# Optimization experiments

Hardware: AMD Instinct MI355X
Metric: run time of the kernel (lower is better)

The kernel has to match this reference:

```python
import math
import jax, jax.numpy as jnp
import numpy as np

DIM = 1280
NUM_HEADS = 16
HEAD_DIM = DIM // NUM_HEADS  # 80
N_SEG = 8
SEG_LEN = 1024
TOTAL = N_SEG * SEG_LEN  # 8192


def setup_inputs() -> dict:
    key = jax.random.key(0)
    ks = jax.random.split(key, 6)
    hidden_states = jax.random.normal(ks[0], (TOTAL, DIM), dtype=jnp.float32)
    # equal-length packed segments (8 images x 1024 patches)
    cu_seqlens = jnp.arange(N_SEG + 1, dtype=jnp.int32) * SEG_LEN
    rotary_pos_emb = jax.random.uniform(ks[1], (TOTAL, HEAD_DIM // 2), dtype=jnp.float32) * (2.0 * math.pi)
    s = 0.02
    qkv_w = jax.random.normal(ks[2], (DIM, 3 * DIM), dtype=jnp.float32) * s
    qkv_b = jnp.zeros((3 * DIM,), dtype=jnp.float32)
    proj_w = jax.random.normal(ks[3], (DIM, DIM), dtype=jnp.float32) * s
    proj_b = jnp.zeros((DIM,), dtype=jnp.float32)
    return {
        "hidden_states": hidden_states,
        "rotary_pos_emb": rotary_pos_emb,
        "qkv_w": qkv_w,
        "qkv_b": qkv_b,
        "proj_w": proj_w,
        "proj_b": proj_b,
        "cu_seqlens": cu_seqlens,
    }


def _rotate_half(x):
    d = x.shape[-1] // 2
    return jnp.concatenate([-x[..., d:], x[..., :d]], axis=-1)


def _apply_rope(t, freqs):
    # t: [S, H, D] ; freqs: [S, D/2]
    orig = t.dtype
    tf = t.astype(jnp.float32)
    cos = jnp.tile(jnp.cos(freqs), (1, 2))[:, None, :].astype(jnp.float32)  # [S,1,D]
    sin = jnp.tile(jnp.sin(freqs), (1, 2))[:, None, :].astype(jnp.float32)
    return (tf * cos + _rotate_half(tf) * sin).astype(orig)


def reference(hidden_states, rotary_pos_emb, qkv_w, qkv_b, proj_w, proj_b, cu_seqlens):
    S, dim = hidden_states.shape
    H, D = NUM_HEADS, HEAD_DIM
    n_seg = cu_seqlens.shape[0] - 1  # static
    L = S // n_seg  # equal-length segments

    qkv = hidden_states @ qkv_w + qkv_b            # [S, 3*dim]
    qkv = qkv.reshape(S, 3, H, D)
    q, k, v = qkv[:, 0], qkv[:, 1], qkv[:, 2]      # [S, H, D]

    q = _apply_rope(q, rotary_pos_emb)
    k = _apply_rope(k, rotary_pos_emb)

    # block-diagonal (per-segment) attention, vectorized over segments
    qs = q.reshape(n_seg, L, H, D).transpose(0, 2, 1, 3)  # [G,H,L,D]
    ks = k.reshape(n_seg, L, H, D).transpose(0, 2, 1, 3)
    vs = v.reshape(n_seg, L, H, D).transpose(0, 2, 1, 3)

    scale = 1.0 / math.sqrt(D)
    scores = jnp.einsum("ghld,ghmd->ghlm", qs, ks) * scale       # [G,H,L,L]
    probs = jax.nn.softmax(scores.astype(jnp.float32), axis=-1).astype(qs.dtype)
    out = jnp.einsum("ghlm,ghmd->ghld", probs, vs)               # [G,H,L,D]
    out = out.transpose(0, 2, 1, 3).reshape(S, H * D)            # [S, dim]
    return out @ proj_w + proj_b
```

## Files before the change

kernel.cpp:

```cpp
#include <hip/hip_runtime.h>
#include <hip/hip_bf16.h>
#include <math.h>

#define DIM 1280
#define NHEADS 16
#define HD 80
#define HDP 96
#define NSEG 8
#define SEGLEN 1024
#define TOTAL (NSEG*SEGLEN)

typedef unsigned short u16;
typedef __attribute__((ext_vector_type(8))) short bf16x8;
typedef __attribute__((ext_vector_type(4))) float f32x4;

__device__ __forceinline__ u16 f2b(float f) {
    union { float f; unsigned int i; } v; v.f = f;
    unsigned int x = v.i;
    unsigned int r = x + 0x7FFFu + ((x >> 16) & 1u);
    return (u16)(r >> 16);
}
__device__ __forceinline__ float b2f(u16 u) {
    union { unsigned int i; float f; } v; v.i = ((unsigned int)u) << 16;
    return v.f;
}
__device__ __forceinline__ void gload16(const u16* g, u16* l) {
    __builtin_amdgcn_global_load_lds(
        (const __attribute__((address_space(1))) unsigned int*)g,
        (__attribute__((address_space(3))) unsigned int*)l, 16, 0, 0);
}

__global__ __launch_bounds__(256) void cvt_f32_bf16(const float* __restrict__ in,
                                                    u16* __restrict__ out, int n4) {
    int i = blockIdx.x * 256 + threadIdx.x;
    if (i >= n4) return;
    float4 a = ((const float4*)in)[i];
    u16 o[4] = { f2b(a.x), f2b(a.y), f2b(a.z), f2b(a.w) };
    *(ulong1*)&out[i*4] = *(ulong1*)o;
}

__global__ __launch_bounds__(256) void cvtT_w(const float* __restrict__ in,
                                              u16* __restrict__ out, int K, int N) {
    __shared__ float t[32][33];
    const int kb = blockIdx.x * 32, nb = blockIdx.y * 32;
    const int tx = threadIdx.x & 31, ty = threadIdx.x >> 5;
    #pragma unroll
    for (int i = 0; i < 4; ++i) {
        int r = i*8 + ty;
        t[r][tx] = in[(size_t)(kb + r)*N + nb + tx];
    }
    __syncthreads();
    #pragma unroll
    for (int i = 0; i < 4; ++i) {
        int n = i*8 + ty;
        out[(size_t)(nb + n)*K + kb + tx] = f2b(t[tx][n]);
    }
}

__global__ __launch_bounds__(256) void ctab_build(const float* __restrict__ rp,
                                                  float2* __restrict__ cs) {
    int i = blockIdx.x * 256 + threadIdx.x;
    if (i >= TOTAL*40) return;
    float s, c;
    sincosf(rp[i], &s, &c);
    cs[i] = make_float2(c, s);
}

template<int MODE>
__global__ __launch_bounds__(512, 2) void gemm8p(
    const u16* __restrict__ A, const u16* __restrict__ BT,
    const float* __restrict__ bias,
    float* __restrict__ Cf, u16* __restrict__ qo, u16* __restrict__ ko,
    u16* __restrict__ vo, int M, int N, int K, int nbx)
{
    __shared__ u16 sA[2][256*64];
    __shared__ u16 sB[2][256*64];

    const int tid = threadIdx.x;
    const int w = tid >> 6, l = tid & 63;
    const int lq = l & 15, lg = l >> 4;
    const int wm = w >> 2, wn = w & 3;

    const int nwg = gridDim.x;
    const int q8 = nwg >> 3;
    const int id = blockIdx.x;
    const int id2 = (id & 7) * q8 + (id >> 3);
    const int bx = id2 % nbx, by = id2 / nbx;
    const int brow = by * 256, bcol = bx * 256;

    const int rlo  = w*8 + (l >> 3);
    const int srcc = (l & 7) ^ ((l >> 3) & 7);
    const size_t aBase = (size_t)(brow + rlo)*K + srcc*8;
    const size_t bBase = (size_t)(bcol + rlo)*K + srcc*8;

    const int cx0 = (0 + lg) ^ (lq & 7);
    const int cx1 = (4 + lg) ^ (lq & 7);

    f32x4 acc[8][4] = {};
    const int NT = K >> 6;

    u16* cA = &sA[0][0]; u16* cB = &sB[0][0];
    u16* nA = &sA[1][0]; u16* nB = &sB[1][0];

    #pragma unroll
    for (int ci = 0; ci < 4; ++ci) {
        gload16(A  + aBase + (size_t)(ci*64)*K, &cA[(ci*512 + w*64)*8]);
        gload16(BT + bBase + (size_t)(ci*64)*K, &cB[(ci*512 + w*64)*8]);
    }
    asm volatile("s_waitcnt vmcnt(0)" ::: "memory");
    __builtin_amdgcn_s_barrier();

    for (int t = 0; t < NT; ++t) {
        const bool pf = (t + 1 < NT);
        const int kb = (t + 1) << 6;
        bf16x8 af[4], bf[4];

        if (pf) {
            gload16(A  + aBase + (size_t)(0*64)*K + kb, &nA[(0*512 + w*64)*8]);
            gload16(A  + aBase + (size_t)(2*64)*K + kb, &nA[(2*512 + w*64)*8]);
            gload16(BT + bBase + (size_t)(0*64)*K + kb, &nB[(0*512 + w*64)*8]);
        }
        #pragma unroll
        for (int n = 0; n < 4; ++n)
            bf[n] = *(const bf16x8*)&cB[(wn*64 + n*16 + lq)*64 + cx0*8];
        #pragma unroll
        for (int mi = 0; mi < 4; ++mi)
            af[mi] = *(const bf16x8*)&cA[(wm*128 + mi*16 + lq)*64 + cx0*8];
        __builtin_amdgcn_s_barrier();
        __builtin_amdgcn_s_setprio(1);
        #pragma unroll
        for (int mi = 0; mi < 4; ++mi)
            #pragma unroll
            for (int n = 0; n < 4; ++n)
                acc[mi][n] = __builtin_amdgcn_mfma_f32_16x16x32_bf16(af[mi], bf[n], acc[mi][n], 0, 0, 0);
        __builtin_amdgcn_s_setprio(0);
        __builtin_amdgcn_s_barrier();

        if (pf) {
            gload16(A  + aBase + (size_t)(1*64)*K + kb, &nA[(1*512 + w*64)*8]);
            gload16(A  + aBase + (size_t)(3*64)*K + kb, &nA[(3*512 + w*64)*8]);
            gload16(BT + bBase + (size_t)(1*64)*K + kb, &nB[(1*512 + w*64)*8]);
        }
        #pragma unroll
        for (int mi = 0; mi < 4; ++mi)
            af[mi] = *(const bf16x8*)&cA[(wm*128 + 64 + mi*16 + lq)*64 + cx0*8];
        __builtin_amdgcn_s_barrier();
        __builtin_amdgcn_s_setprio(1);
        #pragma unroll
        for (int mi = 0; mi < 4; ++mi)
            #pragma unroll
            for (int n = 0; n < 4; ++n)
                acc[4+mi][n] = __builtin_amdgcn_mfma_f32_16x16x32_bf16(af[mi], bf[n], acc[4+mi][n], 0, 0, 0);
        __builtin_amdgcn_s_setprio(0);
        __builtin_amdgcn_s_barrier();

        if (pf) {
            gload16(BT + bBase + (size_t)(2*64)*K + kb, &nB[(2*512 + w*64)*8]);
            gload16(BT + bBase + (size_t)(3*64)*K + kb, &nB[(3*512 + w*64)*8]);
        }
        #pragma unroll
        for (int n = 0; n < 4; ++n)
            bf[n] = *(const bf16x8*)&cB[(wn*64 + n*16 + lq)*64 + cx1*8];
        #pragma unroll
        for (int mi = 0; mi < 4; ++mi)
            af[mi] = *(const bf16x8*)&cA[(wm*128 + mi*16 + lq)*64 + cx1*8];
        __builtin_amdgcn_s_barrier();
        __builtin_amdgcn_s_setprio(1);
        #pragma unroll
        for (int mi = 0; mi < 4; ++mi)
            #pragma unroll
            for (int n = 0; n < 4; ++n)
                acc[mi][n] = __builtin_amdgcn_mfma_f32_16x16x32_bf16(af[mi], bf[n], acc[mi][n], 0, 0, 0);
        __builtin_amdgcn_s_setprio(0);
        __builtin_amdgcn_s_barrier();

        #pragma unroll
        for (int mi = 0; mi < 4; ++mi)
            af[mi] = *(const bf16x8*)&cA[(wm*128 + 64 + mi*16 + lq)*64 + cx1*8];
        __builtin_amdgcn_s_barrier();
        __builtin_amdgcn_s_setprio(1);
        #pragma unroll
        for (int mi = 0; mi < 4; ++mi)
            #pragma unroll
            for (int n = 0; n < 4; ++n)
                acc[4+mi][n] = __builtin_amdgcn_mfma_f32_16x16x32_bf16(af[mi], bf[n], acc[4+mi][n], 0, 0, 0);
        __builtin_amdgcn_s_setprio(0);
        if (pf) asm volatile("s_waitcnt vmcnt(0)" ::: "memory");
        __builtin_amdgcn_s_barrier();

        u16* tA = cA; cA = nA; nA = tA;
        u16* tB = cB; cB = nB; nB = tB;
    }

    #pragma unroll
    for (int mf = 0; mf < 8; ++mf) {
        #pragma unroll
        for (int n = 0; n < 4; ++n) {
            const int col = bcol + wn*64 + n*16 + lq;
            const float bv = bias[col];
            #pragma unroll
            for (int r = 0; r < 4; ++r) {
                const int row = brow + wm*128 + mf*16 + lg*4 + r;
                float val = acc[mf][n][r] + bv;
                if (MODE == 0) {
                    Cf[(size_t)row*N + col] = val;
                } else {
                    int part = col / DIM, rem = col - part*DIM;
                    int hh = rem / HD, dd = rem - hh*HD;
                    int g = row >> 10, ll = row & 1023;
                    size_t tok = (size_t)((g*NHEADS + hh)*SEGLEN + ll);
                    if      (part == 0) qo[tok*HDP + dd] = f2b(val);
                    else if (part == 1) ko[tok*HDP + dd] = f2b(val);
                    else                vo[tok*HD  + dd] = f2b(val);
                }
            }
        }
    }
}

__global__ __launch_bounds__(256) void rope_pad2(u16* __restrict__ qb, u16* __restrict__ kb,
                                                 const float2* __restrict__ cs)
{
    int idx = blockIdx.x * 256 + threadIdx.x;
    int l = idx & 1023, h = (idx >> 10) & 15, g = idx >> 14;
    size_t base = ((size_t)((g*NHEADS + h)*SEGLEN + l)) * HDP;
    const float2* c0 = cs + (size_t)(g*SEGLEN + l) * 40;
    #pragma unroll
    for (int p = 0; p < 5; ++p) {
        float cv[8], sv[8];
        #pragma unroll
        for (int j2 = 0; j2 < 4; ++j2) {
            float4 f = ((const float4*)(c0 + p*8))[j2];
            cv[j2*2] = f.x; sv[j2*2] = f.y; cv[j2*2+1] = f.z; sv[j2*2+1] = f.w;
        }
        bf16x8 qlo = *(const bf16x8*)&qb[base + p*8];
        bf16x8 qhi = *(const bf16x8*)&qb[base + 40 + p*8];
        bf16x8 klo = *(const bf16x8*)&kb[base + p*8];
        bf16x8 khi = *(const bf16x8*)&kb[base + 40 + p*8];
        bf16x8 qlo2, qhi2, klo2, khi2;
        #pragma unroll
        for (int j = 0; j < 8; ++j) {
            float a  = b2f((u16)qlo[j]), b  = b2f((u16)qhi[j]);
            qlo2[j] = (short)f2b(a*cv[j]  - b*sv[j]);
            qhi2[j] = (short)f2b(b*cv[j]  + a*sv[j]);
            float ka = b2f((u16)klo[j]), kb2 = b2f((u16)khi[j]);
            klo2[j] = (short)f2b(ka*cv[j] - kb2*sv[j]);
            khi2[j] = (short)f2b(kb2*cv[j] + ka*sv[j]);
        }
        *(bf16x8*)&qb[base + p*8]      = qlo2;
        *(bf16x8*)&qb[base + 40 + p*8] = qhi2;
        *(bf16x8*)&kb[base + p*8]      = klo2;
        *(bf16x8*)&kb[base + 40 + p*8] = khi2;
    }
    bf16x8 z = {};
    *(bf16x8*)&qb[base + 80] = z; *(bf16x8*)&qb[base + 88] = z;
    *(bf16x8*)&kb[base + 80] = z; *(bf16x8*)&kb[base + 88] = z;
}

__global__ __launch_bounds__(256) void transpose_v(const u16* __restrict__ v,
                                                   u16* __restrict__ vt)
{
    __shared__ u16 sT[64][82];
    const int gh = blockIdx.y;
    const int st = blockIdx.x;
    const u16* src = v  + (size_t)gh*SEGLEN*HD + (size_t)st*64*HD;
    u16*       dst = vt + (size_t)gh*HD*SEGLEN + (size_t)st*64;
    const int tid = threadIdx.x;
    #pragma unroll
    for (int p = 0; p < 20; ++p) {
        int e = p*256 + tid;
        int r = e / 80, c = e - r*80;
        sT[r][c] = src[r*HD + c];
    }
    __syncthreads();
    #pragma unroll
    for (int p = 0; p < 20; ++p) {
        int e = p*256 + tid;
        int dd = e >> 6, s = e & 63;
        dst[(size_t)dd*SEGLEN + s] = sT[s][dd];
    }
}

__global__ __launch_bounds__(256) void attn_mfma(
    const u16* __restrict__ qb, const u16* __restrict__ kb,
    const u16* __restrict__ vt, u16* __restrict__ ob)
{
    const int qt = blockIdx.x;
    const int h  = blockIdx.y;
    const int g  = blockIdx.z;
    const float scale = 0.11180339887498949f;
    const float L2E = 1.4426950408889634f;

    __shared__ u16 sK[64*HDP];
    __shared__ u16 sVT[80][72];
    __shared__ u16 sP[4][16][72];

    const int tid = threadIdx.x;
    const int w = tid >> 6, l = tid & 63;
    const int lq = l & 15, lg = l >> 4;

    const size_t gh = (size_t)(g*NHEADS + h);
    const u16* Qg  = qb + gh*SEGLEN*HDP + (size_t)qt*64*HDP;
    const u16* Kg  = kb + gh*SEGLEN*HDP;
    const u16* VTg = vt + gh*HD*SEGLEN;

    bf16x8 qf[3];
    #pragma unroll
    for (int s = 0; s < 3; ++s)
        qf[s] = *(const bf16x8*)(Qg + (size_t)(w*16 + lq)*HDP + s*32 + lg*8);

    float m = -1e30f, lse = 0.f;
    f32x4 Oc[5] = {};

    for (int kt = 0; kt < 16; ++kt) {
        __syncthreads();
        #pragma unroll
        for (int i = 0; i < 3; ++i) {
            int o = (i*4 + w)*1024 + l*16;
            int row = o / 192, cc = (o % 192) >> 1;
            gload16(Kg + (size_t)(kt*64 + row)*HDP + cc, &sK[(i*4 + w)*512]);
        }
        #pragma unroll
        for (int p = 0; p < 3; ++p) {
            int c = p*256 + tid;
            if (c < 640) {
                int dd = c >> 3, s8 = (c & 7)*8;
                *(bf16x8*)&sVT[dd][s8] =
                    *(const bf16x8*)(VTg + (size_t)dd*SEGLEN + kt*64 + s8);
            }
        }
        __syncthreads();

        f32x4 sf[4];
        #pragma unroll
        for (int fi = 0; fi < 4; ++fi) {
            f32x4 c = {0.f, 0.f, 0.f, 0.f};
            #pragma unroll
            for (int s = 0; s < 3; ++s) {
                bf16x8 a = *(const bf16x8*)&sK[(fi*16 + lq)*HDP + s*32 + lg*8];
                c = __builtin_amdgcn_mfma_f32_16x16x32_bf16(a, qf[s], c, 0, 0, 0);
            }
            sf[fi] = c;
        }

        float sv[4][4];
        float rm = -1e30f;
        #pragma unroll
        for (int fi = 0; fi < 4; ++fi)
            #pragma unroll
            for (int r = 0; r < 4; ++r) {
                float x = sf[fi][r] * scale;
                sv[fi][r] = x;
                rm = fmaxf(rm, x);
            }
        rm = fmaxf(rm, __shfl_xor(rm, 16, 64));
        rm = fmaxf(rm, __shfl_xor(rm, 32, 64));
        float mnew = fmaxf(m, rm);
        float alpha = exp2f((m - mnew) * L2E);
        float psum = 0.f;
        #pragma unroll
        for (int fi = 0; fi < 4; ++fi)
            #pragma unroll
            for (int r = 0; r < 4; ++r) {
                float p = exp2f((sv[fi][r] - mnew) * L2E);
                sv[fi][r] = p;
                psum += p;
            }
        psum += __shfl_xor(psum, 16, 64);
        psum += __shfl_xor(psum, 32, 64);
        lse = lse * alpha + psum;
        m = mnew;

        #pragma unroll
        for (int fi = 0; fi < 4; ++fi) {
            unsigned int w0 = (unsigned int)f2b(sv[fi][0]) | ((unsigned int)f2b(sv[fi][1]) << 16);
            unsigned int w1 = (unsigned int)f2b(sv[fi][2]) | ((unsigned int)f2b(sv[fi][3]) << 16);
            uint2 val; val.x = w0; val.y = w1;
            *(uint2*)&sP[w][lq][fi*16 + lg*4] = val;
        }

        float a0 = __shfl(alpha, lg*4 + 0, 64);
        float a1 = __shfl(alpha, lg*4 + 1, 64);
        float a2 = __shfl(alpha, lg*4 + 2, 64);
        float a3 = __shfl(alpha, lg*4 + 3, 64);
        #pragma unroll
        for (int n = 0; n < 5; ++n) {
            Oc[n][0] *= a0; Oc[n][1] *= a1; Oc[n][2] *= a2; Oc[n][3] *= a3;
        }

        #pragma unroll
        for (int ks = 0; ks < 2; ++ks) {
            bf16x8 pa = *(const bf16x8*)&sP[w][lq][ks*32 + lg*8];
            #pragma unroll
            for (int n = 0; n < 5; ++n) {
                bf16x8 vb = *(const bf16x8*)&sVT[n*16 + lq][ks*32 + lg*8];
                Oc[n] = __builtin_amdgcn_mfma_f32_16x16x32_bf16(pa, vb, Oc[n], 0, 0, 0);
            }
        }
    }

    float inv = 1.f / lse;
    float i0 = __shfl(inv, lg*4 + 0, 64);
    float i1 = __shfl(inv, lg*4 + 1, 64);
    float i2 = __shfl(inv, lg*4 + 2, 64);
    float i3 = __shfl(inv, lg*4 + 3, 64);
    const float iv[4] = { i0, i1, i2, i3 };
    #pragma unroll
    for (int n = 0; n < 5; ++n) {
        #pragma unroll
        for (int r = 0; r < 4; ++r) {
            int tok = g*SEGLEN + qt*64 + w*16 + lg*4 + r;
            int col = h*HD + n*16 + lq;
            ob[(size_t)tok*DIM + col] = f2b(Oc[n][r] * iv[r]);
        }
    }
}

extern "C" void kernel_launch(void* const* d_in, const int* in_sizes, int n_in,
                              void* d_out, int out_size, void* d_ws, size_t ws_size,
                              hipStream_t stream) {
    const float* hs     = (const float*)d_in[0];
    const float* rope   = (const float*)d_in[1];
    const float* qkv_w  = (const float*)d_in[2];
    const float* qkv_b  = (const float*)d_in[3];
    const float* proj_w = (const float*)d_in[4];
    const float* proj_b = (const float*)d_in[5];

    char* ws = (char*)d_ws;
    u16* hsb    = (u16*)(ws);
    u16* wqkvt  = (u16*)(ws + 20971520);
    u16* wprojt = (u16*)(ws + 30801920);
    u16* qpad   = (u16*)(ws + 34078720);
    u16* kpad   = (u16*)(ws + 59244544);
    u16* vbuf   = (u16*)(ws + 84410368);
    u16* vtb    = (u16*)(ws + 105381888);
    u16* obb    = (u16*)(ws + 126353408);
    float2* ctab = (float2*)(ws + 126353408);

    cvt_f32_bf16<<<(TOTAL*DIM/4 + 255)/256, 256, 0, stream>>>(hs, hsb, TOTAL*DIM/4);
    cvtT_w<<<dim3(DIM/32, 3*DIM/32), 256, 0, stream>>>(qkv_w, wqkvt, DIM, 3*DIM);
    cvtT_w<<<dim3(DIM/32, DIM/32), 256, 0, stream>>>(proj_w, wprojt, DIM, DIM);
    ctab_build<<<(TOTAL*40 + 255)/256, 256, 0, stream>>>(rope, ctab);

    gemm8p<1><<<dim3((3*DIM/256) * (TOTAL/256)), 512, 0, stream>>>(
        hsb, wqkvt, qkv_b, nullptr, qpad, kpad, vbuf, TOTAL, 3*DIM, DIM, 3*DIM/256);

    rope_pad2<<<NSEG*NHEADS*SEGLEN/256, 256, 0, stream>>>(qpad, kpad, ctab);

    transpose_v<<<dim3(SEGLEN/64, NSEG*NHEADS), 256, 0, stream>>>(vbuf, vtb);

    attn_mfma<<<dim3(SEGLEN/64, NHEADS, NSEG), 256, 0, stream>>>(qpad, kpad, vtb, obb);

    gemm8p<0><<<dim3((DIM/256) * (TOTAL/256)), 512, 0, stream>>>(
        obb, wprojt, proj_b, (float*)d_out, nullptr, nullptr, nullptr, TOTAL, DIM, DIM, DIM/256);
}
```

Baseline: 441.7 us.

## Fold softmax scale into Q, lazy rescale, swizzled K LDS, packed bf16 cvt

```diff
diff --git a/kernel.cpp b/kernel.cpp
--- a/kernel.cpp
+++ b/kernel.cpp
@@ -14,6 +14,8 @@
 typedef __attribute__((ext_vector_type(8))) short bf16x8;
 typedef __attribute__((ext_vector_type(4))) float f32x4;
 
+#define QSCALE 0.16129841766598387f
+
 __device__ __forceinline__ u16 f2b(float f) {
     union { float f; unsigned int i; } v; v.f = f;
     unsigned int x = v.i;
@@ -28,6 +30,11 @@
     __builtin_amdgcn_global_load_lds(
         (const __attribute__((address_space(1))) unsigned int*)g,
         (__attribute__((address_space(3))) unsigned int*)l, 16, 0, 0);
+}
+__device__ __forceinline__ unsigned int cvt_pk_bf16(float lo, float hi) {
+    unsigned int r;
+    asm("v_cvt_pk_bf16_f32 %0, %1, %2" : "=v"(r) : "v"(lo), "v"(hi));
+    return r;
 }
 
 __global__ __launch_bounds__(256) void cvt_f32_bf16(const float* __restrict__ in,
@@ -116,10 +123,13 @@
         bf16x8 af[4], bf[4];
 
         if (pf) {
-            gload16(A  + aBase + (size_t)(0*64)*K + kb, &nA[(0*512 + w*64)*8]);
-            gload16(A  + aBase + (size_t)(2*64)*K + kb, &nA[(2*512 + w*64)*8]);
-            gload16(BT + bBase + (size_t)(0*64)*K + kb, &nB[(0*512 + w*64)*8]);
-        }
+            #pragma unroll
+            for (int ci = 0; ci < 4; ++ci) {
+                gload16(A  + aBase + (size_t)(ci*64)*K + kb, &nA[(ci*512 + w*64)*8]);
+                gload16(BT + bBase + (size_t)(ci*64)*K + kb, &nB[(ci*512 + w*64)*8]);
+            }
+        }
+
         #pragma unroll
         for (int n = 0; n < 4; ++n)
             bf[n] = *(const bf16x8*)&cB[(wn*64 + n*16 + lq)*64 + cx0*8];
@@ -136,11 +146,6 @@
         __builtin_amdgcn_s_setprio(0);
         __builtin_amdgcn_s_barrier();
 
-        if (pf) {
-            gload16(A  + aBase + (size_t)(1*64)*K + kb, &nA[(1*512 + w*64)*8]);
-            gload16(A  + aBase + (size_t)(3*64)*K + kb, &nA[(3*512 + w*64)*8]);
-            gload16(BT + bBase + (size_t)(1*64)*K + kb, &nB[(1*512 + w*64)*8]);
-        }
         #pragma unroll
         for (int mi = 0; mi < 4; ++mi)
             af[mi] = *(const bf16x8*)&cA[(wm*128 + 64 + mi*16 + lq)*64 + cx0*8];
@@ -154,10 +159,6 @@
         __builtin_amdgcn_s_setprio(0);
         __builtin_amdgcn_s_barrier();
 
-        if (pf) {
-            gload16(BT + bBase + (size_t)(2*64)*K + kb, &nB[(2*512 + w*64)*8]);
-            gload16(BT + bBase + (size_t)(3*64)*K + kb, &nB[(3*512 + w*64)*8]);
-        }
         #pragma unroll
         for (int n = 0; n < 4; ++n)
             bf[n] = *(const bf16x8*)&cB[(wn*64 + n*16 + lq)*64 + cx1*8];
@@ -209,7 +210,7 @@
                     int hh = rem / HD, dd = rem - hh*HD;
                     int g = row >> 10, ll = row & 1023;
                     size_t tok = (size_t)((g*NHEADS + hh)*SEGLEN + ll);
-                    if      (part == 0) qo[tok*HDP + dd] = f2b(val);
+                    if      (part == 0) qo[tok*HDP + dd] = f2b(val * QSCALE);
                     else if (part == 1) ko[tok*HDP + dd] = f2b(val);
                     else                vo[tok*HD  + dd] = f2b(val);
                 }
@@ -288,8 +289,6 @@
     const int qt = blockIdx.x;
     const int h  = blockIdx.y;
     const int g  = blockIdx.z;
-    const float scale = 0.11180339887498949f;
-    const float L2E = 1.4426950408889634f;
 
     __shared__ u16 sK[64*HDP];
     __shared__ u16 sVT[80][72];
@@ -304,6 +303,15 @@
     const u16* Kg  = kb + gh*SEGLEN*HDP;
     const u16* VTg = vt + gh*HD*SEGLEN;
 
+    const int sig_l = l ^ ((l >> 3) & 7);
+    int srow[3], scc[3];
+    #pragma unroll
+    for (int i = 0; i < 3; ++i) {
+        int gi = (i*4 + w)*64 + sig_l;
+        srow[i] = gi / 12;
+        scc[i]  = gi % 12;
+    }
+
     bf16x8 qf[3];
     #pragma unroll
     for (int s = 0; s < 3; ++s)
@@ -315,11 +323,8 @@
     for (int kt = 0; kt < 16; ++kt) {
         __syncthreads();
         #pragma unroll
-        for (int i = 0; i < 3; ++i) {
-            int o = (i*4 + w)*1024 + l*16;
-            int row = o / 192, cc = (o % 192) >> 1;
-            gload16(Kg + (size_t)(kt*64 + row)*HDP + cc, &sK[(i*4 + w)*512]);
-        }
+        for (int i = 0; i < 3; ++i)
+            gload16(Kg + (size_t)(kt*64 + srow[i])*HDP + scc[i]*8, &sK[(i*4 + w)*512]);
         #pragma unroll
         for (int p = 0; p < 3; ++p) {
             int c = p*256 + tid;
@@ -337,7 +342,10 @@
             f32x4 c = {0.f, 0.f, 0.f, 0.f};
             #pragma unroll
             for (int s = 0; s < 3; ++s) {
-                bf16x8 a = *(const bf16x8*)&sK[(fi*16 + lq)*HDP + s*32 + lg*8];
+                int flat = (fi*16 + lq)*12 + s*4 + lg;
+                int c6 = flat & 63;
+                int lc = (flat & ~63) | (c6 ^ ((c6 >> 3) & 7));
+                bf16x8 a = *(const bf16x8*)&sK[lc*8];
                 c = __builtin_amdgcn_mfma_f32_16x16x32_bf16(a, qf[s], c, 0, 0, 0);
             }
             sf[fi] = c;
@@ -349,43 +357,58 @@
         for (int fi = 0; fi < 4; ++fi)
             #pragma unroll
             for (int r = 0; r < 4; ++r) {
-                float x = sf[fi][r] * scale;
+                float x = sf[fi][r];
                 sv[fi][r] = x;
                 rm = fmaxf(rm, x);
             }
         rm = fmaxf(rm, __shfl_xor(rm, 16, 64));
         rm = fmaxf(rm, __shfl_xor(rm, 32, 64));
-        float mnew = fmaxf(m, rm);
-        float alpha = exp2f((m - mnew) * L2E);
-        float psum = 0.f;
-        #pragma unroll
-        for (int fi = 0; fi < 4; ++fi)
-            #pragma unroll
-            for (int r = 0; r < 4; ++r) {
-                float p = exp2f((sv[fi][r] - mnew) * L2E);
-                sv[fi][r] = p;
-                psum += p;
-            }
-        psum += __shfl_xor(psum, 16, 64);
-        psum += __shfl_xor(psum, 32, 64);
-        lse = lse * alpha + psum;
-        m = mnew;
+
+        if (__all(rm <= m + 8.0f)) {
+            float psum = 0.f;
+            #pragma unroll
+            for (int fi = 0; fi < 4; ++fi)
+                #pragma unroll
+                for (int r = 0; r < 4; ++r) {
+                    float p = exp2f(sv[fi][r] - m);
+                    sv[fi][r] = p;
+                    psum += p;
+                }
+            psum += __shfl_xor(psum, 16, 64);
+            psum += __shfl_xor(psum, 32, 64);
+            lse += psum;
+        } else {
+            float mnew = fmaxf(m, rm);
+            float alpha = exp2f(m - mnew);
+            float psum = 0.f;
+            #pragma unroll
+            for (int fi = 0; fi < 4; ++fi)
+                #pragma unroll
+                for (int r = 0; r < 4; ++r) {
+                    float p = exp2f(sv[fi][r] - mnew);
+                    sv[fi][r] = p;
+                    psum += p;
+                }
+            psum += __shfl_xor(psum, 16, 64);
+            psum += __shfl_xor(psum, 32, 64);
+            lse = lse * alpha + psum;
+            m = mnew;
+            float a0 = __shfl(alpha, lg*4 + 0, 64);
+            float a1 = __shfl(alpha, lg*4 + 1, 64);
+            float a2 = __shfl(alpha, lg*4 + 2, 64);
+            float a3 = __shfl(alpha, lg*4 + 3, 64);
+            #pragma unroll
+            for (int n = 0; n < 5; ++n) {
+                Oc[n][0] *= a0; Oc[n][1] *= a1; Oc[n][2] *= a2; Oc[n][3] *= a3;
+            }
+        }
 
         #pragma unroll
         for (int fi = 0; fi < 4; ++fi) {
-            unsigned int w0 = (unsigned int)f2b(sv[fi][0]) | ((unsigned int)f2b(sv[fi][1]) << 16);
-            unsigned int w1 = (unsigned int)f2b(sv[fi][2]) | ((unsigned int)f2b(sv[fi][3]) << 16);
-            uint2 val; val.x = w0; val.y = w1;
+            uint2 val;
+            val.x = cvt_pk_bf16(sv[fi][0], sv[fi][1]);
+            val.y = cvt_pk_bf16(sv[fi][2], sv[fi][3]);
             *(uint2*)&sP[w][lq][fi*16 + lg*4] = val;
-        }
-
-        float a0 = __shfl(alpha, lg*4 + 0, 64);
-        float a1 = __shfl(alpha, lg*4 + 1, 64);
-        float a2 = __shfl(alpha, lg*4 + 2, 64);
-        float a3 = __shfl(alpha, lg*4 + 3, 64);
-        #pragma unroll
-        for (int n = 0; n < 5; ++n) {
-            Oc[n][0] *= a0; Oc[n][1] *= a1; Oc[n][2] *= a2; Oc[n][3] *= a3;
         }
 
         #pragma unroll
```

After: 478.8 us. +8.4%, slower.
